# Performance work log

Measured on AMD Instinct MI355X. Metric: run time of the kernel, lower is better.

Reference implementation:

```python
import jax, jax.numpy as jnp
import numpy as np

B, FEAT, FIELD, K = 16384, 2048, 32, 64

def setup_inputs() -> dict:
    key = jax.random.key(0)
    k1, k2, k3, k4 = jax.random.split(key, 4)
    x = jax.random.normal(k1, (B, FEAT), dtype=jnp.float32)
    # nn.Linear(feature_size, 1): weight [1, FEAT] (use vector), bias [1] (scalar)
    w = jax.random.normal(k2, (FEAT,), dtype=jnp.float32) / np.sqrt(FEAT)
    b = jax.random.normal(k3, (), dtype=jnp.float32)
    # v ~ N(0, 0.01) as in torch.normal(0, 0.01, ...)
    v = 0.01 * jax.random.normal(k4, (FEAT, FIELD, K), dtype=jnp.float32)
    return {"x": x, "w": w, "b": b, "v": v}

def reference(x, w, b, v):
    # linear part: Linear(feature_size, 1).squeeze() -> [B]
    linear_part = x @ w + b  # [B]
    # field_x = tensordot(x, v, dims=1) -> [B, FIELD, K]
    field_x = jnp.einsum('bf,fsk->bsk', x, v)
    # sum_{i<j} sum_k f_i * f_j  ==  0.5 * (||sum_i f_i||^2 - sum_i ||f_i||^2)
    s = field_x.sum(axis=1)                      # [B, K]
    sq = (field_x * field_x).sum(axis=(1, 2))    # [B]
    interaction = 0.5 * ((s * s).sum(axis=-1) - sq)  # [B]
    return jax.nn.sigmoid(linear_part + interaction)
```

## Files before the change

kernel.cpp:

```cpp
#include <hip/hip_runtime.h>
#include <cstdint>
#include <cstddef>

#define B_ROWS 16384
#define FEAT   2048
#define FIELD  32
#define KDIM   64
#define NCOLS  2048
#define NAUG   2176

using half8   = __attribute__((ext_vector_type(8))) _Float16;
using half4   = __attribute__((ext_vector_type(4))) _Float16;
using floatx4 = __attribute__((ext_vector_type(4))) float;

__device__ __forceinline__ void load_lds16(const void* g, void* l) {
  __builtin_amdgcn_global_load_lds((const __attribute__((address_space(1))) void*)g,
                                   (__attribute__((address_space(3))) void*)l, 16, 0, 0);
}

__global__ __launch_bounds__(256) void k_cvt_x(const float* __restrict__ x,
                                               _Float16* __restrict__ xh) {
  size_t i = (size_t)(blockIdx.x * 256 + threadIdx.x) * 8;
  float4 v0 = *(const float4*)(x + i);
  float4 v1 = *(const float4*)(x + i + 4);
  half8 h = { (_Float16)v0.x, (_Float16)v0.y, (_Float16)v0.z, (_Float16)v0.w,
              (_Float16)v1.x, (_Float16)v1.y, (_Float16)v1.z, (_Float16)v1.w };
  *(half8*)(xh + i) = h;
}

__global__ __launch_bounds__(256) void k_prep(const float* __restrict__ v,
                                              const float* __restrict__ w,
                                              _Float16* __restrict__ vt) {
  const int bb = blockIdx.x;
  const int t = threadIdx.x;
  if (bb < 1024) {
    __shared__ _Float16 tile[64 * 68];
    const int f0 = (bb >> 5) * 64;
    const int n0 = (bb & 31) * 64;
#pragma unroll
    for (int j = 0; j < 4; ++j) {
      int c = j * 256 + t;
      int row = c >> 4;
      int col = (c & 15) * 4;
      float4 val = *(const float4*)(v + (size_t)(f0 + row) * NCOLS + n0 + col);
      tile[row * 68 + col + 0] = (_Float16)val.x;
      tile[row * 68 + col + 1] = (_Float16)val.y;
      tile[row * 68 + col + 2] = (_Float16)val.z;
      tile[row * 68 + col + 3] = (_Float16)val.w;
    }
    __syncthreads();
#pragma unroll
    for (int j = 0; j < 4; ++j) {
      int c = j * 256 + t;
      int nl = c >> 4;
      int fl = (c & 15) * 4;
      half4 h = { tile[(fl + 0) * 68 + nl], tile[(fl + 1) * 68 + nl],
                  tile[(fl + 2) * 68 + nl], tile[(fl + 3) * 68 + nl] };
      *(half4*)(vt + (size_t)(n0 + nl) * FEAT + f0 + fl) = h;
    }
  } else if (bb < 1536) {
    const int k = t & 63;
    const int f = (bb - 1024) * 4 + (t >> 6);
    float s = 0.f;
#pragma unroll
    for (int si = 0; si < FIELD; ++si) s += v[(size_t)f * NCOLS + si * KDIM + k];
    vt[(size_t)(NCOLS + k) * FEAT + f] = (_Float16)s;
  } else {
    int idx = (bb - 1536) * 256 + t;
    int r = NCOLS + KDIM + (idx >> 11);
    int f = idx & 2047;
    vt[(size_t)r * FEAT + f] = (r == NCOLS + KDIM) ? (_Float16)w[f] : (_Float16)0.f;
  }
}

__global__ __launch_bounds__(256) void k_gemm(const _Float16* __restrict__ xh,
                                              const _Float16* __restrict__ vt,
                                              float* __restrict__ arg) {
  __shared__ __align__(16) _Float16 lds_a[128 * 64];
  __shared__ __align__(16) _Float16 lds_b[128 * 64];
  const int t = threadIdx.x;
  const int n0 = blockIdx.x * 128;
  const int m0 = blockIdx.y * 128;
  const int lane = t & 63;
  const int wave = t >> 6;
  const int wm = (wave & 1) * 64;
  const int wn = (wave >> 1) * 64;
  const int lr = lane & 15;
  const int lk = (lane >> 4) * 8;

  floatx4 acc[4][4] = {};

  for (int k0 = 0; k0 < FEAT; k0 += 64) {
#pragma unroll
    for (int i = 0; i < 4; ++i) {
      int c = i * 256 + t;
      int row = c >> 3;
      int g = (c & 7) ^ (row & 7);
      load_lds16(xh + (size_t)(m0 + row) * FEAT + k0 + g * 8, lds_a + c * 8);
      load_lds16(vt + (size_t)(n0 + row) * FEAT + k0 + g * 8, lds_b + c * 8);
    }
    __syncthreads();
#pragma unroll
    for (int ks = 0; ks < 64; ks += 32) {
      const int kc = (ks + lk) >> 3;
      half8 af[4], bf[4];
#pragma unroll
      for (int f = 0; f < 4; ++f) {
        int ma = wm + f * 16 + lr;
        int nb = wn + f * 16 + lr;
        af[f] = *(const half8*)(lds_a + ma * 64 + (kc ^ (ma & 7)) * 8);
        bf[f] = *(const half8*)(lds_b + nb * 64 + (kc ^ (nb & 7)) * 8);
      }
#pragma unroll
      for (int fm = 0; fm < 4; ++fm)
#pragma unroll
        for (int fn = 0; fn < 4; ++fn)
          acc[fm][fn] = __builtin_amdgcn_mfma_f32_16x16x32_f16(af[fm], bf[fn],
                                                               acc[fm][fn], 0, 0, 0);
    }
    __syncthreads();
  }

  const int cq = lane >> 4;
#pragma unroll
  for (int fm = 0; fm < 4; ++fm) {
#pragma unroll
    for (int r = 0; r < 4; ++r) {
      float contrib = 0.f;
#pragma unroll
      for (int fn = 0; fn < 4; ++fn) {
        int col = n0 + wn + fn * 16 + lr;
        float vv = acc[fm][fn][r];
        float q = vv * vv;
        if (col < NCOLS)                contrib -= 0.5f * q;
        else if (col < NCOLS + KDIM)    contrib += 0.5f * q;
        else if (col == NCOLS + KDIM)   contrib += vv;
      }
      contrib += __shfl_xor(contrib, 1);
      contrib += __shfl_xor(contrib, 2);
      contrib += __shfl_xor(contrib, 4);
      contrib += __shfl_xor(contrib, 8);
      if (lr == 0) atomicAdd(&arg[m0 + wm + fm * 16 + cq * 4 + r], contrib);
    }
  }
}

__global__ __launch_bounds__(256) void k_fin(const float* __restrict__ arg,
                                             const float* __restrict__ b,
                                             float* __restrict__ out) {
  int i = blockIdx.x * 256 + threadIdx.x;
  float z = arg[i] + b[0];
  out[i] = 1.f / (1.f + __expf(-z));
}

extern "C" void kernel_launch(void* const* d_in, const int* in_sizes, int n_in,
                              void* d_out, int out_size, void* d_ws, size_t ws_size,
                              hipStream_t stream) {
  const float* x = (const float*)d_in[0];
  const float* w = (const float*)d_in[1];
  const float* b = (const float*)d_in[2];
  const float* v = (const float*)d_in[3];
  float* out = (float*)d_out;

  char* ws = (char*)d_ws;
  _Float16* xh  = (_Float16*)ws;
  _Float16* vt  = (_Float16*)(ws + 67108864);
  float*    arg = (float*)(ws + 67108864 + 8912896);

  hipMemsetAsync(arg, 0, B_ROWS * sizeof(float), stream);
  k_cvt_x<<<16384, 256, 0, stream>>>(x, xh);
  k_prep<<<2048, 256, 0, stream>>>(v, w, vt);
  k_gemm<<<dim3(17, 128), 256, 0, stream>>>(xh, vt, arg);
  k_fin<<<64, 256, 0, stream>>>(arg, b, out);
}
```

Before: 416.7 us.

## Merge x conversion, v prep and arg zeroing into one kernel; swap GEMM grid order

```diff
diff --git a/kernel.cpp b/kernel.cpp
--- a/kernel.cpp
+++ b/kernel.cpp
@@ -18,25 +18,31 @@
                                    (__attribute__((address_space(3))) void*)l, 16, 0, 0);
 }
 
-__global__ __launch_bounds__(256) void k_cvt_x(const float* __restrict__ x,
-                                               _Float16* __restrict__ xh) {
-  size_t i = (size_t)(blockIdx.x * 256 + threadIdx.x) * 8;
-  float4 v0 = *(const float4*)(x + i);
-  float4 v1 = *(const float4*)(x + i + 4);
-  half8 h = { (_Float16)v0.x, (_Float16)v0.y, (_Float16)v0.z, (_Float16)v0.w,
-              (_Float16)v1.x, (_Float16)v1.y, (_Float16)v1.z, (_Float16)v1.w };
-  *(half8*)(xh + i) = h;
-}
-
-__global__ __launch_bounds__(256) void k_prep(const float* __restrict__ v,
+__global__ __launch_bounds__(256) void k_prep(const float* __restrict__ x,
+                                              const float* __restrict__ v,
                                               const float* __restrict__ w,
-                                              _Float16* __restrict__ vt) {
+                                              _Float16* __restrict__ xh,
+                                              _Float16* __restrict__ vt,
+                                              float* __restrict__ arg) {
   const int bb = blockIdx.x;
   const int t = threadIdx.x;
-  if (bb < 1024) {
+  if (bb < 8192) {
+    size_t i = ((size_t)bb * 256 + t) * 16;
+    float4 v0 = *(const float4*)(x + i);
+    float4 v1 = *(const float4*)(x + i + 4);
+    float4 v2 = *(const float4*)(x + i + 8);
+    float4 v3 = *(const float4*)(x + i + 12);
+    half8 h0 = { (_Float16)v0.x, (_Float16)v0.y, (_Float16)v0.z, (_Float16)v0.w,
+                 (_Float16)v1.x, (_Float16)v1.y, (_Float16)v1.z, (_Float16)v1.w };
+    half8 h1 = { (_Float16)v2.x, (_Float16)v2.y, (_Float16)v2.z, (_Float16)v2.w,
+                 (_Float16)v3.x, (_Float16)v3.y, (_Float16)v3.z, (_Float16)v3.w };
+    *(half8*)(xh + i) = h0;
+    *(half8*)(xh + i + 8) = h1;
+  } else if (bb < 9216) {
     __shared__ _Float16 tile[64 * 68];
-    const int f0 = (bb >> 5) * 64;
-    const int n0 = (bb & 31) * 64;
+    const int b2 = bb - 8192;
+    const int f0 = (b2 >> 5) * 64;
+    const int n0 = (b2 & 31) * 64;
 #pragma unroll
     for (int j = 0; j < 4; ++j) {
       int c = j * 256 + t;
@@ -58,18 +64,20 @@
                   tile[(fl + 2) * 68 + nl], tile[(fl + 3) * 68 + nl] };
       *(half4*)(vt + (size_t)(n0 + nl) * FEAT + f0 + fl) = h;
     }
-  } else if (bb < 1536) {
+  } else if (bb < 9728) {
     const int k = t & 63;
-    const int f = (bb - 1024) * 4 + (t >> 6);
+    const int f = (bb - 9216) * 4 + (t >> 6);
     float s = 0.f;
 #pragma unroll
     for (int si = 0; si < FIELD; ++si) s += v[(size_t)f * NCOLS + si * KDIM + k];
     vt[(size_t)(NCOLS + k) * FEAT + f] = (_Float16)s;
-  } else {
-    int idx = (bb - 1536) * 256 + t;
+  } else if (bb < 10240) {
+    int idx = (bb - 9728) * 256 + t;
     int r = NCOLS + KDIM + (idx >> 11);
     int f = idx & 2047;
     vt[(size_t)r * FEAT + f] = (r == NCOLS + KDIM) ? (_Float16)w[f] : (_Float16)0.f;
+  } else {
+    arg[(bb - 10240) * 256 + t] = 0.f;
   }
 }
 
@@ -79,8 +87,8 @@
   __shared__ __align__(16) _Float16 lds_a[128 * 64];
   __shared__ __align__(16) _Float16 lds_b[128 * 64];
   const int t = threadIdx.x;
-  const int n0 = blockIdx.x * 128;
-  const int m0 = blockIdx.y * 128;
+  const int m0 = blockIdx.x * 128;
+  const int n0 = blockIdx.y * 128;
   const int lane = t & 63;
   const int wave = t >> 6;
   const int wm = (wave & 1) * 64;
@@ -167,9 +175,7 @@
   _Float16* vt  = (_Float16*)(ws + 67108864);
   float*    arg = (float*)(ws + 67108864 + 8912896);
 
-  hipMemsetAsync(arg, 0, B_ROWS * sizeof(float), stream);
-  k_cvt_x<<<16384, 256, 0, stream>>>(x, xh);
-  k_prep<<<2048, 256, 0, stream>>>(v, w, vt);
-  k_gemm<<<dim3(17, 128), 256, 0, stream>>>(xh, vt, arg);
+  k_prep<<<10304, 256, 0, stream>>>(x, v, w, xh, vt, arg);
+  k_gemm<<<dim3(128, 17), 256, 0, stream>>>(xh, vt, arg);
   k_fin<<<64, 256, 0, stream>>>(arg, b, out);
 }
```

After: 409.6 us. No clear change (-1.7%).
